# Kernel optimization log

Measured on AMD Instinct MI355X. Metric: run time of the kernel, lower is better.

Reference implementation:

```python
import jax, jax.numpy as jnp
import numpy as np

MIMO_RANK = 4  # module constant; q/k are identical across rank and mimo_v=mimo_out=ones,
               # q_bias=k_bias=0, so the rank sum equals MIMO_RANK * single-rank output.


def _rotary(t, ang):
    # split-half rotary: t [..., d], ang [..., d//2]
    d2 = t.shape[-1] // 2
    t1, t2 = t[..., :d2], t[..., d2:]
    c, s = jnp.cos(ang), jnp.sin(ang)
    return jnp.concatenate([t1 * c - t2 * s, t1 * s + t2 * c], axis=-1)


def setup_inputs() -> dict:
    key = jax.random.key(0)
    ks = jax.random.split(key, 6)
    b, l, h, dv, g, dqk = 2, 4096, 32, 64, 1, 128
    x = jax.random.normal(ks[0], (b, l, h, dv), jnp.float32)
    # positive step sizes (discretization dt)
    dt = jax.random.uniform(ks[1], (b, l, h), jnp.float32) * 0.05 + 1e-3
    # negative decay rates so exp(A*dt) < 1
    A = -(jax.random.uniform(ks[2], (h,), jnp.float32) + 0.5)
    B_gate = jax.random.normal(ks[3], (b, l, g, dqk), jnp.float32)
    C_gate = jax.random.normal(ks[4], (b, l, g, dqk), jnp.float32)
    D = jax.random.normal(ks[5], (h,), jnp.float32)
    return {"x": x, "dt": dt, "A": A, "B_gate": B_gate, "C_gate": C_gate,
            "D": D, "chunk_size": 64}


def reference(x, dt, A, B_gate, C_gate, D, chunk_size):
    # Mamba3 MIMO chunked selective scan (SSD) with rotary QK decay.
    # Recurrence per (b, h):  H_t = exp(A_h*dt_t) * H_{t-1} + rot(k_t) (dt_t x_t)^T
    #                         y_t = rot(q_t)^T H_t * MIMO_RANK + D_h * x_t
    # where q=C_gate, k=B_gate (shared across heads, ngroups=1) and the rotary
    # angle is theta_t = cumsum(dt) (TILELANG_ROTARY_DIV=2 -> dqk//2 angles).
    b, l, h, dv = x.shape
    dqk = C_gate.shape[-1]
    c = chunk_size
    n = l // c

    ang = jnp.cumsum(dt, axis=1)[..., None]                     # [b,l,h,1]
    ang = jnp.broadcast_to(ang, (b, l, h, dqk // 2))
    q = jnp.broadcast_to(C_gate[:, :, 0, :][:, :, None, :], (b, l, h, dqk))
    k = jnp.broadcast_to(B_gate[:, :, 0, :][:, :, None, :], (b, l, h, dqk))
    rotq = _rotary(q, ang)                                      # [b,l,h,dqk]
    rotk = _rotary(k, ang)
    adt = A[None, None, :] * dt                                 # [b,l,h] log-decay

    chunk = lambda t: t.reshape(b, n, c, *t.shape[2:])
    rq, rk = chunk(rotq), chunk(rotk)                           # [b,n,c,h,dqk]
    u = chunk(dt[..., None] * x)                                # [b,n,c,h,dv]
    a = chunk(adt)                                              # [b,n,c,h]
    cum = jnp.cumsum(a, axis=2)                                 # within-chunk cum log-decay

    # ---- intra-chunk (quadratic within chunk) ----
    seg = cum[:, :, :, None, :] - cum[:, :, None, :, :]         # [b,n,t,s,h]
    mask = jnp.tril(jnp.ones((c, c), bool))
    L = jnp.where(mask[None, None, :, :, None], jnp.exp(seg), 0.0)
    S = jnp.einsum('bnthd,bnshd->bntsh', rq, rk)                # [b,n,t,s,h]
    y_intra = jnp.einsum('bntsh,bnshe->bnthe', S * L, u)        # [b,n,c,h,dv]

    # ---- inter-chunk state recurrence ----
    decay_to_end = jnp.exp(cum[:, :, -1:, :] - cum)             # [b,n,c,h]
    dH = jnp.einsum('bnshd,bnsh,bnshe->bnhde', rk, decay_to_end, u)  # [b,n,h,dqk,dv]
    cdecay = jnp.exp(cum[:, :, -1, :])                          # [b,n,h] full-chunk decay

    def step(H, inp):
        dc, dh = inp
        Hprev = H
        return dc[:, :, None, None] * H + dh, Hprev

    H0 = jnp.zeros((b, h, dqk, dv), x.dtype)
    _, Hprev = jax.lax.scan(step, H0,
                            (jnp.moveaxis(cdecay, 1, 0), jnp.moveaxis(dH, 1, 0)))
    Hprev = jnp.moveaxis(Hprev, 0, 1)                           # [b,n,h,dqk,dv]

    y_inter = jnp.einsum('bnthd,bnth,bnhde->bnthe', rq, jnp.exp(cum), Hprev)

    y = MIMO_RANK * (y_intra + y_inter).reshape(b, l, h, dv)
    return y + D[None, None, :, None] * x
```

## Files before the change

kernel.cpp:

```cpp
#include <hip/hip_runtime.h>
#include <hip/hip_bf16.h>

#define BB 2
#define LL 4096
#define HH 32
#define DV 64
#define DQK 128
#define CC 64
#define NN 64
#define MIMO_RANK 4.0f

typedef __attribute__((ext_vector_type(8))) short short8;
typedef __attribute__((ext_vector_type(4))) float f32x4;

__device__ __forceinline__ ushort f2bf(float f) {
    uint u = __float_as_uint(f);
    u += 0x7FFF + ((u >> 16) & 1);
    return (ushort)(u >> 16);
}
__device__ __forceinline__ float bfbits2f(uint lo16) {
    return __uint_as_float(lo16 << 16);
}
__device__ __forceinline__ uint pkbf2(float lo, float hi) {
    return (uint)f2bf(lo) | ((uint)f2bf(hi) << 16);
}
union U8 { uint u[4]; short8 s; };

__device__ __forceinline__ int rk_off(int s, int d) {
    return s * 128 + (((((d >> 3) & 15) ^ (s & 7)) << 3)) + (d & 7);
}
__device__ __forceinline__ int uwT_off(int e, int s) {
    return e * 64 + ((((s >> 3) ^ (e & 7)) & 7) << 3) + (s & 7);
}
__device__ __forceinline__ int fSL(int t) {
    return (((t & 3) << 1) ^ ((t >> 2) & 7)) & 7;
}
__device__ __forceinline__ int SL_off(int t, int s) {
    return t * 64 + ((((s >> 3) ^ fSL(t)) & 7) << 3) + (s & 7);
}

__device__ __forceinline__ void make_rot_frags(const float* __restrict__ G,
                                               size_t gb, float cv, float sv,
                                               int kgrp, short8* fr) {
    #pragma unroll
    for (int kk = 0; kk < 4; ++kk) {
        int d0 = kk * 32 + kgrp;
        int dl = d0 & 63;
        bool low = d0 < 64;
        float4 a1 = *(const float4*)(G + gb + dl);
        float4 b1 = *(const float4*)(G + gb + dl + 4);
        float4 a2 = *(const float4*)(G + gb + dl + 64);
        float4 b2 = *(const float4*)(G + gb + dl + 68);
        float v0, v1, v2, v3, v4, v5, v6, v7;
        if (low) {
            v0 = a1.x * cv - a2.x * sv; v1 = a1.y * cv - a2.y * sv;
            v2 = a1.z * cv - a2.z * sv; v3 = a1.w * cv - a2.w * sv;
            v4 = b1.x * cv - b2.x * sv; v5 = b1.y * cv - b2.y * sv;
            v6 = b1.z * cv - b2.z * sv; v7 = b1.w * cv - b2.w * sv;
        } else {
            v0 = a1.x * sv + a2.x * cv; v1 = a1.y * sv + a2.y * cv;
            v2 = a1.z * sv + a2.z * cv; v3 = a1.w * sv + a2.w * cv;
            v4 = b1.x * sv + b2.x * cv; v5 = b1.y * sv + b2.y * cv;
            v6 = b1.z * sv + b2.z * cv; v7 = b1.w * sv + b2.w * cv;
        }
        U8 r;
        r.u[0] = pkbf2(v0, v1); r.u[1] = pkbf2(v2, v3);
        r.u[2] = pkbf2(v4, v5); r.u[3] = pkbf2(v6, v7);
        fr[kk] = r.s;
    }
}

__global__ __launch_bounds__(256) void k_scan_dt(const float* __restrict__ dt,
                                                 const float* __restrict__ A,
                                                 float4* __restrict__ tbl,
                                                 float* __restrict__ cdecay) {
    int bh = blockIdx.x;
    int b = bh / HH, h = bh % HH;
    int tid = threadIdx.x;
    const int PT = LL / 256;
    float v[PT];
    float s = 0.f;
    int tbase = tid * PT;
    for (int i = 0; i < PT; ++i) {
        v[i] = dt[(((size_t)b * LL + tbase + i) * HH) + h];
        s += v[i];
    }
    int lane = tid & 63, wv = tid >> 6;
    float ps = s;
    for (int off = 1; off < 64; off <<= 1) {
        float o = __shfl_up(ps, off, 64);
        if (lane >= off) ps += o;
    }
    __shared__ float wsum[4];
    if (lane == 63) wsum[wv] = ps;
    __syncthreads();
    float wadd = 0.f;
    for (int w = 0; w < wv; ++w) wadd += wsum[w];
    float run0 = wadd + ps - s;
    float run_end = run0 + s;
    float aend  = __shfl(run_end, lane | 3, 64);
    float aprev = __shfl(run0, lane & ~3, 64);
    float Ah = A[h];
    if ((tid & 3) == 0) {
        int n = tid >> 2;
        cdecay[(b * NN + n) * HH + h] = __expf(Ah * (aend - aprev));
    }
    float4* tb = tbl + ((size_t)(b * HH + h) * LL) + tbase;
    float run = run0;
    for (int i = 0; i < PT; ++i) {
        run += v[i];
        float sv, cv;
        __sincosf(run, &sv, &cv);
        float dw = __expf(Ah * (aend - run));
        float et = __expf(Ah * (run - aend));
        tb[i] = make_float4(cv, sv, v[i] * dw, et);
    }
}

__global__ __launch_bounds__(256, 3) void k_intra(
    const float* __restrict__ x, const float* __restrict__ Bg,
    const float* __restrict__ Cg, const float4* __restrict__ tbl,
    const float* __restrict__ Dd,
    float* __restrict__ out, ushort* __restrict__ dH) {
    int n = blockIdx.x, h = blockIdx.y, b = blockIdx.z;
    int tid = threadIdx.x;
    int t0 = n * CC;

    __shared__ ushort rkS[CC * DQK];
    __shared__ ushort uwT[DV * CC];

    int wv = tid >> 6, lane = tid & 63;
    int lrow = lane & 15;
    int g = lane >> 4;
    int kgrp = g * 8;
    int orow = g * 4;

    const float4* tb = tbl + ((size_t)(b * HH + h) * LL) + t0;
    const float* BgRow = Bg + ((size_t)b * LL + t0) * DQK;

    float4 bg0[2], bg1[2], bg2[2], bg3[2], tvS[2];
    #pragma unroll
    for (int it = 0; it < 2; ++it) {
        int w = tid + 256 * it;
        int s = w >> 3, oct = w & 7;
        const float* p = BgRow + s * DQK + 8 * oct;
        bg0[it] = *(const float4*)(p);
        bg1[it] = *(const float4*)(p + 4);
        bg2[it] = *(const float4*)(p + 64);
        bg3[it] = *(const float4*)(p + 68);
        tvS[it] = tb[s];
    }
    float xv[2][8], dwv[2][8];
    #pragma unroll
    for (int it = 0; it < 2; ++it) {
        int w = tid + 256 * it;
        int e = w & 63;
        int s0 = 8 * (w >> 6);
        #pragma unroll
        for (int j = 0; j < 8; ++j) {
            xv[it][j] = x[((((size_t)b * LL + t0 + s0 + j) * HH) + h) * DV + e];
            dwv[it][j] = tb[s0 + j].z;
        }
    }

    int t_own = 16 * wv + lrow;
    float4 tq = tb[t_own];
    short8 aq[4];
    make_rot_frags(Cg, ((size_t)b * LL + t0 + t_own) * DQK, tq.x, tq.y, kgrp, aq);

    #pragma unroll
    for (int it = 0; it < 2; ++it) {
        int w = tid + 256 * it;
        int s = w >> 3, oct = w & 7;
        float cv = tvS[it].x, sv = tvS[it].y;
        U8 lo, hi;
        lo.u[0] = pkbf2(bg0[it].x * cv - bg2[it].x * sv, bg0[it].y * cv - bg2[it].y * sv);
        lo.u[1] = pkbf2(bg0[it].z * cv - bg2[it].z * sv, bg0[it].w * cv - bg2[it].w * sv);
        lo.u[2] = pkbf2(bg1[it].x * cv - bg3[it].x * sv, bg1[it].y * cv - bg3[it].y * sv);
        lo.u[3] = pkbf2(bg1[it].z * cv - bg3[it].z * sv, bg1[it].w * cv - bg3[it].w * sv);
        hi.u[0] = pkbf2(bg0[it].x * sv + bg2[it].x * cv, bg0[it].y * sv + bg2[it].y * cv);
        hi.u[1] = pkbf2(bg0[it].z * sv + bg2[it].z * cv, bg0[it].w * sv + bg2[it].w * cv);
        hi.u[2] = pkbf2(bg1[it].x * sv + bg3[it].x * cv, bg1[it].y * sv + bg3[it].y * cv);
        hi.u[3] = pkbf2(bg1[it].z * sv + bg3[it].z * cv, bg1[it].w * sv + bg3[it].w * cv);
        *(short8*)&rkS[rk_off(s, 8 * oct)] = lo.s;
        *(short8*)&rkS[rk_off(s, 8 * oct + 64)] = hi.s;
    }
    #pragma unroll
    for (int it = 0; it < 2; ++it) {
        int w = tid + 256 * it;
        int e = w & 63;
        int s0 = 8 * (w >> 6);
        U8 pk;
        #pragma unroll
        for (int jp = 0; jp < 4; ++jp) {
            pk.u[jp] = pkbf2(xv[it][2 * jp] * dwv[it][2 * jp],
                             xv[it][2 * jp + 1] * dwv[it][2 * jp + 1]);
        }
        *(short8*)&uwT[uwT_off(e, s0)] = pk.s;
    }

    __syncthreads();

    f32x4 accS[4] = {{0.f,0.f,0.f,0.f},{0.f,0.f,0.f,0.f},
                     {0.f,0.f,0.f,0.f},{0.f,0.f,0.f,0.f}};
    #pragma unroll
    for (int kk = 0; kk < 4; ++kk) {
        #pragma unroll
        for (int nt = 0; nt < 4; ++nt) {
            int s = 16 * nt + lrow;
            const short8 bfr = *(const short8*)&rkS[rk_off(s, 32 * kk + kgrp)];
            accS[nt] = __builtin_amdgcn_mfma_f32_16x16x32_bf16(
                aq[kk], bfr, accS[nt], 0, 0, 0);
        }
    }

    short8 aH[2][2];
    #pragma unroll
    for (int kk = 0; kk < 2; ++kk) {
        #pragma unroll
        for (int mt = 0; mt < 2; ++mt) {
            int d = 32 * wv + 16 * mt + lrow;
            uint vv[8];
            #pragma unroll
            for (int j = 0; j < 8; ++j)
                vv[j] = rkS[rk_off(32 * kk + kgrp + j, d)];
            U8 pk;
            pk.u[0] = vv[0] | (vv[1] << 16);
            pk.u[1] = vv[2] | (vv[3] << 16);
            pk.u[2] = vv[4] | (vv[5] << 16);
            pk.u[3] = vv[6] | (vv[7] << 16);
            aH[kk][mt] = pk.s;
        }
    }

    __syncthreads();

    ushort* SLs = rkS;
    #pragma unroll
    for (int rr = 0; rr < 4; ++rr) {
        int t = 16 * wv + orow + rr;
        float etv = tb[t].w;
        #pragma unroll
        for (int nt = 0; nt < 4; ++nt) {
            int s = 16 * nt + lrow;
            float v = (t >= s) ? accS[nt][rr] * etv : 0.f;
            SLs[SL_off(t, s)] = f2bf(v);
        }
    }

    __syncthreads();

    {
        f32x4 accY[4] = {{0.f,0.f,0.f,0.f},{0.f,0.f,0.f,0.f},
                         {0.f,0.f,0.f,0.f},{0.f,0.f,0.f,0.f}};
        #pragma unroll
        for (int kk = 0; kk < 2; ++kk) {
            const short8 a = *(const short8*)&SLs[SL_off(16 * wv + lrow, 32 * kk + kgrp)];
            #pragma unroll
            for (int nt = 0; nt < 4; ++nt) {
                const short8 bfr = *(const short8*)&uwT[uwT_off(16 * nt + lrow, 32 * kk + kgrp)];
                accY[nt] = __builtin_amdgcn_mfma_f32_16x16x32_bf16(
                    a, bfr, accY[nt], 0, 0, 0);
            }
        }
        float Dh = Dd[h];
        #pragma unroll
        for (int nt = 0; nt < 4; ++nt) {
            int e = 16 * nt + lrow;
            #pragma unroll
            for (int rr = 0; rr < 4; ++rr) {
                int t = 16 * wv + orow + rr;
                size_t oidx = ((((size_t)b * LL + t0 + t) * HH) + h) * DV + e;
                out[oidx] = MIMO_RANK * accY[nt][rr] + Dh * x[oidx];
            }
        }
    }

    {
        f32x4 accH[2][4] = {{{0.f,0.f,0.f,0.f},{0.f,0.f,0.f,0.f},
                             {0.f,0.f,0.f,0.f},{0.f,0.f,0.f,0.f}},
                            {{0.f,0.f,0.f,0.f},{0.f,0.f,0.f,0.f},
                             {0.f,0.f,0.f,0.f},{0.f,0.f,0.f,0.f}}};
        #pragma unroll
        for (int kk = 0; kk < 2; ++kk) {
            #pragma unroll
            for (int mt = 0; mt < 2; ++mt) {
                #pragma unroll
                for (int nt = 0; nt < 4; ++nt) {
                    const short8 bfr = *(const short8*)&uwT[uwT_off(16 * nt + lrow, 32 * kk + kgrp)];
                    accH[mt][nt] = __builtin_amdgcn_mfma_f32_16x16x32_bf16(
                        aH[kk][mt], bfr, accH[mt][nt], 0, 0, 0);
                }
            }
        }
        ushort* dHp = dH + (((size_t)(b * NN + n) * HH) + h) * (DQK * DV);
        #pragma unroll
        for (int q = 0; q < 4; ++q) {
            int mt = q >> 1, np = q & 1;
            U8 st;
            st.u[0] = pkbf2(accH[mt][2 * np][0], accH[mt][2 * np][1]);
            st.u[1] = pkbf2(accH[mt][2 * np][2], accH[mt][2 * np][3]);
            st.u[2] = pkbf2(accH[mt][2 * np + 1][0], accH[mt][2 * np + 1][1]);
            st.u[3] = pkbf2(accH[mt][2 * np + 1][2], accH[mt][2 * np + 1][3]);
            *(short8*)(dHp + ((size_t)(wv * 4 + q) * 64 + lane) * 8) = st.s;
        }
    }
}

__global__ __launch_bounds__(256) void k_scan_chunks(
    uint* __restrict__ dH, const float* __restrict__ cdecay) {
    uint f = blockIdx.x * 256 + threadIdx.x;
    int b = (int)(f >> 17);
    uint r = f & 0x1FFFF;
    int h = (int)((r >> 12) & 31);
    uint base = ((uint)b << 23) | r;
    const float* cd = cdecay + (size_t)b * NN * HH + h;
    float h0 = 0.f, h1 = 0.f;
    for (int n = 0; n < NN; ++n) {
        uint a = base + ((uint)n << 17);
        uint v = dH[a];
        float v0 = bfbits2f(v & 0xFFFF), v1 = bfbits2f(v >> 16);
        dH[a] = pkbf2(h0, h1);
        float c = cd[n * HH];
        h0 = c * h0 + v0;
        h1 = c * h1 + v1;
    }
}

__global__ __launch_bounds__(256, 6) void k_inter(
    const float* __restrict__ Cg, const float4* __restrict__ tbl,
    const float* __restrict__ cdecay, const ushort* __restrict__ Hprev,
    float* __restrict__ out) {
    int n = blockIdx.x, h = blockIdx.y, b = blockIdx.z;
    int tid = threadIdx.x;
    int t0 = n * CC;

    __shared__ __align__(16) uint Hp[16 * 260];

    const float4* tb = tbl + ((size_t)(b * HH + h) * LL) + t0;
    float cdec = cdecay[(b * NN + n) * HH + h];

    const uint* Hsrc = (const uint*)(Hprev + (((size_t)(b * NN + n) * HH) + h) * (DQK * DV));
    #pragma unroll
    for (int it = 0; it < 4; ++it) {
        int p = tid + 256 * it;
        uint4 v = *(const uint4*)(Hsrc + (size_t)p * 4);
        int row = p >> 6, c = p & 63;
        uint4* Hrow = (uint4*)&Hp[row * 260];
        Hrow[c] = v;
    }

    int wv = tid >> 6, lane = tid & 63;
    int lrow = lane & 15;
    int g2 = lane >> 4;
    int kgrp = g2 * 8;
    int orow = g2 * 4;

    int t_own = 16 * wv + lrow;
    float4 tq = tb[t_own];
    short8 aq[4];
    make_rot_frags(Cg, ((size_t)b * LL + t0 + t_own) * DQK, tq.x, tq.y, kgrp, aq);
    __syncthreads();

    f32x4 accI[4] = {{0.f,0.f,0.f,0.f},{0.f,0.f,0.f,0.f},
                     {0.f,0.f,0.f,0.f},{0.f,0.f,0.f,0.f}};
    int mt = g2 >> 1;
    int gp0 = 2 * (g2 & 1);
    #pragma unroll
    for (int kk = 0; kk < 4; ++kk) {
        #pragma unroll
        for (int nt = 0; nt < 4; ++nt) {
            int q = mt * 2 + (nt >> 1);
            int row = kk * 4 + q;
            int sb = (nt & 1) * 2;
            const uint2 u0 = *(const uint2*)&Hp[row * 260 + (16 * gp0 + lrow) * 4 + sb];
            const uint2 u1 = *(const uint2*)&Hp[row * 260 + (16 * (gp0 + 1) + lrow) * 4 + sb];
            U8 fr;
            fr.u[0] = u0.x; fr.u[1] = u0.y; fr.u[2] = u1.x; fr.u[3] = u1.y;
            accI[nt] = __builtin_amdgcn_mfma_f32_16x16x32_bf16(
                aq[kk], fr.s, accI[nt], 0, 0, 0);
        }
    }

    #pragma unroll
    for (int rr = 0; rr < 4; ++rr) {
        int t = 16 * wv + orow + rr;
        float g4 = MIMO_RANK * tb[t].w * cdec;
        #pragma unroll
        for (int nt = 0; nt < 4; ++nt) {
            int e = 16 * nt + lrow;
            size_t oidx = ((((size_t)b * LL + t0 + t) * HH) + h) * DV + e;
            out[oidx] += g4 * accI[nt][rr];
        }
    }
}

extern "C" void kernel_launch(void* const* d_in, const int* in_sizes, int n_in,
                              void* d_out, int out_size, void* d_ws,
                              size_t ws_size, hipStream_t stream) {
    (void)in_sizes; (void)n_in; (void)out_size; (void)ws_size;
    const float* x  = (const float*)d_in[0];
    const float* dt = (const float*)d_in[1];
    const float* A  = (const float*)d_in[2];
    const float* Bg = (const float*)d_in[3];
    const float* Cg = (const float*)d_in[4];
    const float* Dd = (const float*)d_in[5];
    float* out = (float*)d_out;
    float* ws  = (float*)d_ws;

    float4* tbl    = (float4*)ws;
    float*  cdecay = ws + (size_t)BB * HH * LL * 4;
    ushort* dH     = (ushort*)(cdecay + BB * NN * HH);

    k_scan_dt<<<BB * HH, 256, 0, stream>>>(dt, A, tbl, cdecay);
    k_intra<<<dim3(NN, HH, BB), 256, 0, stream>>>(x, Bg, Cg, tbl, Dd, out, dH);
    k_scan_chunks<<<(BB * HH * DQK * DV / 2) / 256, 256, 0, stream>>>(
        (uint*)dH, cdecay);
    k_inter<<<dim3(NN, HH, BB), 256, 0, stream>>>(Cg, tbl, cdecay, dH, out);
}
```

Before: 116.9 us.

## Stage x and decay table into LDS via direct global-to-LDS loads

```diff
diff --git a/kernel.cpp b/kernel.cpp
--- a/kernel.cpp
+++ b/kernel.cpp
@@ -128,6 +128,8 @@
 
     __shared__ ushort rkS[CC * DQK];
     __shared__ ushort uwT[DV * CC];
+    __shared__ float4 tblLds[CC];
+    __shared__ float  xraw[CC * DV];
 
     int wv = tid >> 6, lane = tid & 63;
     int lrow = lane & 15;
@@ -135,44 +137,46 @@
     int kgrp = g * 8;
     int orow = g * 4;
 
-    const float4* tb = tbl + ((size_t)(b * HH + h) * LL) + t0;
     const float* BgRow = Bg + ((size_t)b * LL + t0) * DQK;
 
-    float4 bg0[2], bg1[2], bg2[2], bg3[2], tvS[2];
+    {
+        const float4* tbsrc = tbl + ((size_t)(b * HH + h) * LL) + t0 + lane;
+        __builtin_amdgcn_global_load_lds((const void*)tbsrc, (void*)tblLds,
+                                         16, 0, 0);
+    }
+    #pragma unroll
+    for (int i = 0; i < 4; ++i) {
+        int row = 16 * wv + 4 * i + (lane >> 4);
+        const float* xsrc = x + ((((size_t)b * LL + t0 + row) * HH) + h) * DV
+                            + 4 * (lane & 15);
+        __builtin_amdgcn_global_load_lds((const void*)xsrc,
+                                         (void*)(xraw + (16 * wv + 4 * i) * DV),
+                                         16, 0, 0);
+    }
+    float4 bg0[2], bg1[2], bg2[2], bg3[2];
     #pragma unroll
     for (int it = 0; it < 2; ++it) {
-        int w = tid + 256 * it;
-        int s = w >> 3, oct = w & 7;
+        int s = (tid >> 3) + 32 * it, oct = tid & 7;
         const float* p = BgRow + s * DQK + 8 * oct;
         bg0[it] = *(const float4*)(p);
         bg1[it] = *(const float4*)(p + 4);
         bg2[it] = *(const float4*)(p + 64);
         bg3[it] = *(const float4*)(p + 68);
-        tvS[it] = tb[s];
-    }
-    float xv[2][8], dwv[2][8];
-    #pragma unroll
-    for (int it = 0; it < 2; ++it) {
-        int w = tid + 256 * it;
-        int e = w & 63;
-        int s0 = 8 * (w >> 6);
-        #pragma unroll
-        for (int j = 0; j < 8; ++j) {
-            xv[it][j] = x[((((size_t)b * LL + t0 + s0 + j) * HH) + h) * DV + e];
-            dwv[it][j] = tb[s0 + j].z;
-        }
-    }
+    }
+
+    asm volatile("s_waitcnt vmcnt(0)" ::: "memory");
+    __builtin_amdgcn_sched_barrier(0);
 
     int t_own = 16 * wv + lrow;
-    float4 tq = tb[t_own];
+    float4 tq = tblLds[t_own];
     short8 aq[4];
     make_rot_frags(Cg, ((size_t)b * LL + t0 + t_own) * DQK, tq.x, tq.y, kgrp, aq);
 
     #pragma unroll
     for (int it = 0; it < 2; ++it) {
-        int w = tid + 256 * it;
-        int s = w >> 3, oct = w & 7;
-        float cv = tvS[it].x, sv = tvS[it].y;
+        int s = (tid >> 3) + 32 * it, oct = tid & 7;
+        float4 tv = tblLds[s];
+        float cv = tv.x, sv = tv.y;
         U8 lo, hi;
         lo.u[0] = pkbf2(bg0[it].x * cv - bg2[it].x * sv, bg0[it].y * cv - bg2[it].y * sv);
         lo.u[1] = pkbf2(bg0[it].z * cv - bg2[it].z * sv, bg0[it].w * cv - bg2[it].w * sv);
@@ -185,16 +189,18 @@
         *(short8*)&rkS[rk_off(s, 8 * oct)] = lo.s;
         *(short8*)&rkS[rk_off(s, 8 * oct + 64)] = hi.s;
     }
+
     #pragma unroll
     for (int it = 0; it < 2; ++it) {
-        int w = tid + 256 * it;
-        int e = w & 63;
-        int s0 = 8 * (w >> 6);
+        int s0 = 16 * wv + 8 * it;
+        int e = lane;
         U8 pk;
         #pragma unroll
         for (int jp = 0; jp < 4; ++jp) {
-            pk.u[jp] = pkbf2(xv[it][2 * jp] * dwv[it][2 * jp],
-                             xv[it][2 * jp + 1] * dwv[it][2 * jp + 1]);
+            int sa = s0 + 2 * jp, sb = sa + 1;
+            float xa = xraw[sa * DV + e] * tblLds[sa].z;
+            float xb = xraw[sb * DV + e] * tblLds[sb].z;
+            pk.u[jp] = pkbf2(xa, xb);
         }
         *(short8*)&uwT[uwT_off(e, s0)] = pk.s;
     }
@@ -239,7 +245,7 @@
     #pragma unroll
     for (int rr = 0; rr < 4; ++rr) {
         int t = 16 * wv + orow + rr;
-        float etv = tb[t].w;
+        float etv = tblLds[t].w;
         #pragma unroll
         for (int nt = 0; nt < 4; ++nt) {
             int s = 16 * nt + lrow;
@@ -271,7 +277,7 @@
             for (int rr = 0; rr < 4; ++rr) {
                 int t = 16 * wv + orow + rr;
                 size_t oidx = ((((size_t)b * LL + t0 + t) * HH) + h) * DV + e;
-                out[oidx] = MIMO_RANK * accY[nt][rr] + Dh * x[oidx];
+                out[oidx] = MIMO_RANK * accY[nt][rr] + Dh * xraw[t * DV + e];
             }
         }
     }
```

Result: faster. 113.7 us (-2.7%).
